# Kernel tuning notes

Measured on AMD Instinct MI355X. Metric: run time of the kernel, lower is better.

The kernel has to match this reference:

```python
import jax, jax.numpy as jnp
import numpy as np

M, C, K, D = 2048, 16, 8, 256  # queries, classes, clusters/class, feature_dim
H1, H2 = D, D // 2             # MLP hidden sizes


def setup_inputs() -> dict:
    key = jax.random.key(0)
    ks = jax.random.split(key, 8)
    s1 = 1.0 / np.sqrt(2 * D)
    s2 = 1.0 / np.sqrt(H1)
    s3 = 1.0 / np.sqrt(H2)
    return {
        "query_features": jax.random.normal(ks[0], (M, D), jnp.float32),
        "prototypes": jax.random.normal(ks[1], (C, K, D), jnp.float32),
        "W1": jax.random.normal(ks[2], (2 * D, H1), jnp.float32) * s1,
        "b1": jnp.zeros((H1,), jnp.float32),
        "W2": jax.random.normal(ks[3], (H1, H2), jnp.float32) * s2,
        "b2": jnp.zeros((H2,), jnp.float32),
        "W3": jax.random.normal(ks[4], (H2, 1), jnp.float32) * s3,
        "b3": jnp.zeros((1,), jnp.float32),
    }


def reference(query_features, prototypes, W1, b1, W2, b2, W3, b3):
    # Attention MLP on concat([query, prototype]) for every (query, class, cluster)
    # pair. Split W1 into the query half and prototype half so we never
    # materialize the [M,C,K,2D] concat; broadcast-add instead.
    d = query_features.shape[-1]
    Wq, Wp = W1[:d], W1[d:]
    qh = query_features @ Wq                      # [M, H1]
    ph = jnp.einsum('ckd,dh->ckh', prototypes, Wp)  # [C, K, H1]
    h = jax.nn.relu(qh[:, None, None, :] + ph[None] + b1)   # [M, C, K, H1]
    h = jax.nn.relu(h @ W2 + b2)                              # [M, C, K, H2]
    scores = (h @ W3)[..., 0] + b3[0]                         # [M, C, K]
    attn = jax.nn.softmax(scores, axis=-1)                    # softmax over clusters
    weighted = jnp.einsum('mck,ckd->mcd', attn, prototypes)   # [M, C, D]
    diff = query_features[:, None, :] - weighted              # [M, C, D]
    distances = jnp.sqrt(jnp.sum(diff * diff, axis=-1))       # [M, C]
    return -distances
```

## Files before the change

kernel.cpp:

```cpp
#include <hip/hip_runtime.h>
#include <hip/hip_fp16.h>
#include <cstdint>

typedef __attribute__((ext_vector_type(8))) _Float16 f16x8;
typedef __attribute__((ext_vector_type(4))) float f32x4;
typedef __attribute__((ext_vector_type(16))) float f32x16;

__device__ __forceinline__ f16x8 cvt8(float4 x, float4 y) {
    f16x8 r;
    r[0] = (_Float16)x.x; r[1] = (_Float16)x.y; r[2] = (_Float16)x.z; r[3] = (_Float16)x.w;
    r[4] = (_Float16)y.x; r[5] = (_Float16)y.y; r[6] = (_Float16)y.z; r[7] = (_Float16)y.w;
    return r;
}

__device__ __forceinline__ f16x8 relu8(f16x8 v) {
    f16x8 z = {};
    return __builtin_elementwise_max(v, z);
}

__global__ __launch_bounds__(256)
void xpose(const float* __restrict__ query,
           const float* __restrict__ prot,
           const float* __restrict__ W1,
           const float* __restrict__ W2,
           const float* __restrict__ b2,
           _Float16* __restrict__ w1t,
           f16x8* __restrict__ w2p,
           float* __restrict__ Gm,
           float* __restrict__ q2) {
    int b = blockIdx.x, t = threadIdx.x;
    if (b < 32) {
        __shared__ _Float16 lt[64][73];
        int bi = b >> 2, bj = b & 3;
        int r0 = bi * 64, c0 = bj * 64;
        #pragma unroll
        for (int it = 0; it < 4; ++it) {
            int row = it * 16 + (t >> 4);
            int c4 = (t & 15) * 4;
            float4 v = *(const float4*)(W1 + (r0 + row) * 256 + c0 + c4);
            lt[row][c4]     = (_Float16)v.x;
            lt[row][c4 + 1] = (_Float16)v.y;
            lt[row][c4 + 2] = (_Float16)v.z;
            lt[row][c4 + 3] = (_Float16)v.w;
        }
        __syncthreads();
        int c = t >> 2, kq = t & 3;
        unsigned short o[16];
        #pragma unroll
        for (int i = 0; i < 16; ++i) {
            union { _Float16 f; unsigned short s; } u;
            u.f = lt[kq * 16 + i][c];
            o[i] = u.s;
        }
        _Float16* dst = w1t + (r0 >= 256 ? 65536 : 0) + (c0 + c) * 256 + (r0 & 255) + kq * 16;
        *(uint4*)dst       = *(uint4*)&o[0];
        *(uint4*)(dst + 8) = *(uint4*)&o[8];
    } else if (b < 49) {
        int chunk = (b - 32) * 256 + t;
        int ks = chunk >> 8, h = (chunk >> 7) & 1, c = chunk & 127;
        f16x8 o = {};
        if (ks < 16) {
            #pragma unroll
            for (int j = 0; j < 8; ++j)
                o[j] = (_Float16)W2[(ks * 16 + h * 8 + j) * 128 + c];
        } else if (h == 0) {
            o[0] = (_Float16)b2[c];
        }
        w2p[chunk] = o;
    } else if (b < 81) {
        int pid = (b - 49) * 32 + (t >> 3), l8 = t & 7;
        int c = pid >> 6, k = (pid >> 3) & 7, kp = pid & 7;
        const float4* pa = (const float4*)(prot + (c * 8 + k) * 256 + l8 * 32);
        const float4* pb = (const float4*)(prot + (c * 8 + kp) * 256 + l8 * 32);
        float s = 0.f;
        #pragma unroll
        for (int i = 0; i < 8; ++i) {
            float4 x = pa[i], y = pb[i];
            s += x.x * y.x + x.y * y.y + x.z * y.z + x.w * y.w;
        }
        s += __shfl_xor(s, 1); s += __shfl_xor(s, 2); s += __shfl_xor(s, 4);
        if (l8 == 0) Gm[pid] = s;
    } else {
        int m = (b - 81) * 32 + (t >> 3), l8 = t & 7;
        const float4* qp = (const float4*)(query + m * 256 + l8 * 32);
        float s = 0.f;
        #pragma unroll
        for (int i = 0; i < 8; ++i) {
            float4 x = qp[i];
            s += x.x * x.x + x.y * x.y + x.z * x.z + x.w * x.w;
        }
        s += __shfl_xor(s, 1); s += __shfl_xor(s, 2); s += __shfl_xor(s, 4);
        if (l8 == 0) q2[m] = s;
    }
}

__global__ __launch_bounds__(256, 2)
void prepg(const float* __restrict__ query,
           const float* __restrict__ prot,
           const _Float16* __restrict__ w1t,
           const float* __restrict__ b1,
           _Float16* __restrict__ qh16,
           float* __restrict__ sqp,
           _Float16* __restrict__ phpk) {
    int b = blockIdx.x, t = threadIdx.x;
    int w = t >> 6, l = t & 63, l15 = l & 15, l4 = l >> 4;
    int mode, row0, col0;
    if (b < 128)      { mode = 0; row0 = (b >> 2) * 64;         col0 = (b & 3) * 64; }
    else if (b < 192) { mode = 1; row0 = ((b - 128) >> 1) * 64; col0 = ((b - 128) & 1) * 64; }
    else              { mode = 2; row0 = ((b - 192) >> 2) * 64; col0 = ((b - 192) & 3) * 64; }
    const float* Asrc = (mode == 2) ? prot : query;
    const _Float16* Bsrc = (mode == 2) ? (w1t + 65536) : w1t;

    f32x4 acc[4];
    #pragma unroll
    for (int nt = 0; nt < 4; ++nt) acc[nt] = (f32x4){0.f, 0.f, 0.f, 0.f};

    for (int ks = 0; ks < 8; ++ks) {
        int row = row0 + w * 16 + l15;
        const float* ap = Asrc + row * 256 + ks * 32 + l4 * 8;
        f16x8 af = cvt8(*(const float4*)ap, *(const float4*)(ap + 4));
        f16x8 bf[4];
        #pragma unroll
        for (int nt = 0; nt < 4; ++nt) {
            int col = col0 + nt * 16 + l15;
            if (mode == 1) {
                const float* bp = prot + col * 256 + ks * 32 + l4 * 8;
                bf[nt] = cvt8(*(const float4*)bp, *(const float4*)(bp + 4));
            } else {
                bf[nt] = *(const f16x8*)(Bsrc + col * 256 + ks * 32 + l4 * 8);
            }
        }
        #pragma unroll
        for (int nt = 0; nt < 4; ++nt)
            acc[nt] = __builtin_amdgcn_mfma_f32_16x16x32_f16(af, bf[nt], acc[nt], 0, 0, 0);
    }
    #pragma unroll
    for (int nt = 0; nt < 4; ++nt)
        #pragma unroll
        for (int j = 0; j < 4; ++j) {
            int row = row0 + w * 16 + l4 * 4 + j;
            int col = col0 + nt * 16 + l15;
            float v = acc[nt][j];
            if (mode == 0)      qh16[row * 256 + col] = (_Float16)v;
            else if (mode == 1) sqp[row * 128 + col] = v;
            else                phpk[(((col >> 4) * 2 + ((col >> 3) & 1)) * 128 + row) * 8
                                     + (col & 7)] = (_Float16)(v + b1[col]);
        }
}

__global__ __launch_bounds__(512, 1)
void fused2(const _Float16* __restrict__ qh16,
            const _Float16* __restrict__ phpk,
            const uint4* __restrict__ w2p,
            const float* __restrict__ sqp,
            const float* __restrict__ q2,
            const float* __restrict__ Gm,
            const float* __restrict__ W3,
            float* __restrict__ out) {
    __shared__ uint4 w2l[4352];
    __shared__ float w3l[128];
    __shared__ float spart[2][2][2][128];

    int t = threadIdx.x;
    int wid = t >> 6, l = t & 63;
    int rg = wid & 3, cs = wid >> 2;
    int lk = l & 31, h = l >> 5;
    int ck = rg * 32 + lk;

    for (int i = t; i < 4352; i += 512) w2l[i] = w2p[i];
    if (t < 128) w3l[t] = W3[t];

    f16x8 ph[16];
    #pragma unroll
    for (int ks = 0; ks < 16; ++ks)
        ph[ks] = *(const f16x8*)(phpk + ((ks * 2 + h) * 128 + ck) * 8);

    __syncthreads();

    const _Float16* w2lh = (const _Float16*)w2l;
    int m0 = blockIdx.x * 8;

    for (int mi = 0; mi < 4; ++mi) {
        int mA = m0 + mi * 2;
        const _Float16* qra = qh16 + mA * 256 + h * 8;
        const _Float16* qrb = qra + 256;

        f32x16 acc[2][2];
        #pragma unroll
        for (int mm = 0; mm < 2; ++mm)
            #pragma unroll
            for (int ct = 0; ct < 2; ++ct) acc[mm][ct] = (f32x16){};

        f16x8 qa[4], qb[4];
        #pragma unroll
        for (int p = 0; p < 4; ++p) {
            qa[p] = *(const f16x8*)(qra + p * 16);
            qb[p] = *(const f16x8*)(qrb + p * 16);
        }

        #pragma unroll
        for (int ks = 0; ks < 16; ++ks) {
            f16x8 aA = relu8(qa[ks & 3] + ph[ks]);
            f16x8 aB = relu8(qb[ks & 3] + ph[ks]);
            if (ks < 12) {
                qa[ks & 3] = *(const f16x8*)(qra + (ks + 4) * 16);
                qb[ks & 3] = *(const f16x8*)(qrb + (ks + 4) * 16);
            }
            #pragma unroll
            for (int ct = 0; ct < 2; ++ct) {
                f16x8 bfr = *(const f16x8*)(w2lh + ((ks * 2 + h) * 128 + cs * 64 + ct * 32 + lk) * 8);
                acc[0][ct] = __builtin_amdgcn_mfma_f32_32x32x16_f16(bfr, aA, acc[0][ct], 0, 0, 0);
                acc[1][ct] = __builtin_amdgcn_mfma_f32_32x32x16_f16(bfr, aB, acc[1][ct], 0, 0, 0);
            }
        }
        {
            f16x8 e = {};
            if (h == 0) e[0] = (_Float16)1.0f;
            #pragma unroll
            for (int ct = 0; ct < 2; ++ct) {
                f16x8 bfr = *(const f16x8*)(w2lh + ((32 + h) * 128 + cs * 64 + ct * 32 + lk) * 8);
                acc[0][ct] = __builtin_amdgcn_mfma_f32_32x32x16_f16(bfr, e, acc[0][ct], 0, 0, 0);
                acc[1][ct] = __builtin_amdgcn_mfma_f32_32x32x16_f16(bfr, e, acc[1][ct], 0, 0, 0);
            }
        }

        int buf = mi & 1;
        #pragma unroll
        for (int mm = 0; mm < 2; ++mm) {
            float s = 0.f;
            #pragma unroll
            for (int ct = 0; ct < 2; ++ct)
                #pragma unroll
                for (int r = 0; r < 16; ++r)
                    s = fmaf(fmaxf(acc[mm][ct][r], 0.f),
                             w3l[cs * 64 + ct * 32 + (r & 3) + 8 * (r >> 2) + 4 * h], s);
            s += __shfl_xor(s, 32);
            if (l < 32) spart[buf][mm][cs][ck] = s;
        }
        __syncthreads();

        if (t < 256) {
            int msel = t >> 7, ckk = t & 127, kk = t & 7;
            int m = mA + msel;
            int c = ckk >> 3;
            float s = spart[buf][msel][0][ckk] + spart[buf][msel][1][ckk];
            float mx = s;
            mx = fmaxf(mx, __shfl_xor(mx, 1));
            mx = fmaxf(mx, __shfl_xor(mx, 2));
            mx = fmaxf(mx, __shfl_xor(mx, 4));
            float e = __expf(s - mx);
            float den = e;
            den += __shfl_xor(den, 1); den += __shfl_xor(den, 2); den += __shfl_xor(den, 4);
            float a = e / den;
            float p2 = a * sqp[m * 128 + ckk];
            float p3 = 0.f;
            #pragma unroll
            for (int kq = 0; kq < 8; ++kq) {
                float ak = __shfl(a, (l & 56) | kq);
                p3 = fmaf(ak, Gm[c * 64 + kq * 8 + kk], p3);
            }
            p3 *= a;
            float pr = p3 - 2.f * p2;
            pr += __shfl_xor(pr, 1); pr += __shfl_xor(pr, 2); pr += __shfl_xor(pr, 4);
            if (kk == 0)
                out[m * 16 + c] = -sqrtf(fmaxf(q2[m] + pr, 0.f));
        }
    }
}

extern "C" void kernel_launch(void* const* d_in, const int* in_sizes, int n_in,
                              void* d_out, int out_size, void* d_ws, size_t ws_size,
                              hipStream_t stream) {
    const float* query = (const float*)d_in[0];
    const float* prot  = (const float*)d_in[1];
    const float* W1    = (const float*)d_in[2];
    const float* b1    = (const float*)d_in[3];
    const float* W2    = (const float*)d_in[4];
    const float* b2    = (const float*)d_in[5];
    const float* W3    = (const float*)d_in[6];

    char* ws = (char*)d_ws;
    _Float16* qh16 = (_Float16*)(ws);
    _Float16* w1t  = (_Float16*)(ws + 1048576);
    f16x8*    w2p  = (f16x8*)(ws + 1310720);
    _Float16* phpk = (_Float16*)(ws + 1380352);
    float*    sqp  = (float*)(ws + 1445888);
    float*    q2   = (float*)(ws + 2494464);
    float*    Gm   = (float*)(ws + 2502656);
    float* out = (float*)d_out;

    xpose<<<145, 256, 0, stream>>>(query, prot, W1, W2, b2, w1t, w2p, Gm, q2);
    prepg<<<200, 256, 0, stream>>>(query, prot, w1t, b1, qh16, sqp, phpk);
    fused2<<<256, 512, 0, stream>>>(qh16, phpk, (const uint4*)w2p,
                                    sqp, q2, Gm, W3, out);
}
```

Measured before the change: 47.18 us.

## Merge three kernels into one cooperative kernel with grid-wide syncs

Combines the preprocessing, projection GEMM and fused MLP/softmax/distance kernels into a single cooperative kernel launched with 256 blocks of 512 threads. Each block runs two former 256-thread work units side by side in the first two phases, and grid.sync() separates the phases. Shared memory is reused across phases through a union. The goal is to remove the launch and drain gaps between kernels. The cost is two grid-wide barriers, and the early phases now run under the register budget of the 512-thread MLP phase.

Result: slower. 114.9 us (+143.6%).

```diff
diff --git a/kernel.cpp b/kernel.cpp
--- a/kernel.cpp
+++ b/kernel.cpp
@@ -1,6 +1,9 @@
 #include <hip/hip_runtime.h>
 #include <hip/hip_fp16.h>
+#include <hip/hip_cooperative_groups.h>
 #include <cstdint>
+
+namespace cg = cooperative_groups;
 
 typedef __attribute__((ext_vector_type(8))) _Float16 f16x8;
 typedef __attribute__((ext_vector_type(4))) float f32x4;
@@ -18,252 +21,253 @@
     return __builtin_elementwise_max(v, z);
 }
 
-__global__ __launch_bounds__(256)
-void xpose(const float* __restrict__ query,
-           const float* __restrict__ prot,
-           const float* __restrict__ W1,
-           const float* __restrict__ W2,
-           const float* __restrict__ b2,
-           _Float16* __restrict__ w1t,
-           f16x8* __restrict__ w2p,
-           float* __restrict__ Gm,
-           float* __restrict__ q2) {
-    int b = blockIdx.x, t = threadIdx.x;
-    if (b < 32) {
-        __shared__ _Float16 lt[64][73];
-        int bi = b >> 2, bj = b & 3;
-        int r0 = bi * 64, c0 = bj * 64;
+__global__ __launch_bounds__(512, 1)
+void mega(const float* __restrict__ query, const float* __restrict__ prot,
+          const float* __restrict__ W1, const float* __restrict__ b1,
+          const float* __restrict__ W2, const float* __restrict__ b2,
+          const float* __restrict__ W3,
+          _Float16* __restrict__ qh16, _Float16* __restrict__ w1t,
+          uint4* __restrict__ w2p, _Float16* __restrict__ phpk,
+          float* __restrict__ sqp, float* __restrict__ q2,
+          float* __restrict__ Gm, float* __restrict__ out)
+{
+    __shared__ union SMem {
+        struct { _Float16 lt[2][64][73]; } a;
+        struct { uint4 w2l[4352]; float w3l[128]; float spart[2][2][2][128]; } c;
+    } sm;
+
+    cg::grid_group grid = cg::this_grid();
+    const int t = threadIdx.x;
+
+    {
+        int u = (int)blockIdx.x * 2 + (t >> 8);
+        int tt = t & 255;
+        if (u < 32) {
+            _Float16 (*lt)[73] = sm.a.lt[t >> 8];
+            int bi = u >> 2, bj = u & 3;
+            int r0 = bi * 64, c0 = bj * 64;
+            #pragma unroll
+            for (int it = 0; it < 4; ++it) {
+                int row = it * 16 + (tt >> 4);
+                int c4 = (tt & 15) * 4;
+                float4 v = *(const float4*)(W1 + (r0 + row) * 256 + c0 + c4);
+                lt[row][c4]     = (_Float16)v.x;
+                lt[row][c4 + 1] = (_Float16)v.y;
+                lt[row][c4 + 2] = (_Float16)v.z;
+                lt[row][c4 + 3] = (_Float16)v.w;
+            }
+            __syncthreads();
+            int c = tt >> 2, kq = tt & 3;
+            unsigned short o[16];
+            #pragma unroll
+            for (int i = 0; i < 16; ++i) {
+                union { _Float16 f; unsigned short s; } uu;
+                uu.f = lt[kq * 16 + i][c];
+                o[i] = uu.s;
+            }
+            _Float16* dst = w1t + (r0 >= 256 ? 65536 : 0) + (c0 + c) * 256 + (r0 & 255) + kq * 16;
+            *(uint4*)dst       = *(uint4*)&o[0];
+            *(uint4*)(dst + 8) = *(uint4*)&o[8];
+        } else if (u < 49) {
+            int chunk = (u - 32) * 256 + tt;
+            int ks = chunk >> 8, h = (chunk >> 7) & 1, c = chunk & 127;
+            f16x8 o = {};
+            if (ks < 16) {
+                #pragma unroll
+                for (int j = 0; j < 8; ++j)
+                    o[j] = (_Float16)W2[(ks * 16 + h * 8 + j) * 128 + c];
+            } else if (h == 0) {
+                o[0] = (_Float16)b2[c];
+            }
+            ((f16x8*)w2p)[chunk] = o;
+        } else if (u < 81) {
+            int pid = (u - 49) * 32 + (tt >> 3), l8 = tt & 7;
+            int c = pid >> 6, k = (pid >> 3) & 7, kp = pid & 7;
+            const float4* pa = (const float4*)(prot + (c * 8 + k) * 256 + l8 * 32);
+            const float4* pb = (const float4*)(prot + (c * 8 + kp) * 256 + l8 * 32);
+            float s = 0.f;
+            #pragma unroll
+            for (int i = 0; i < 8; ++i) {
+                float4 x = pa[i], y = pb[i];
+                s += x.x * y.x + x.y * y.y + x.z * y.z + x.w * y.w;
+            }
+            s += __shfl_xor(s, 1); s += __shfl_xor(s, 2); s += __shfl_xor(s, 4);
+            if (l8 == 0) Gm[pid] = s;
+        } else if (u < 145) {
+            int m = (u - 81) * 32 + (tt >> 3), l8 = tt & 7;
+            const float4* qp = (const float4*)(query + m * 256 + l8 * 32);
+            float s = 0.f;
+            #pragma unroll
+            for (int i = 0; i < 8; ++i) {
+                float4 x = qp[i];
+                s += x.x * x.x + x.y * x.y + x.z * x.z + x.w * x.w;
+            }
+            s += __shfl_xor(s, 1); s += __shfl_xor(s, 2); s += __shfl_xor(s, 4);
+            if (l8 == 0) q2[m] = s;
+        }
+    }
+
+    grid.sync();
+
+    {
+        int hu = (int)blockIdx.x * 2 + (t >> 8);
+        if (hu < 200) {
+            int tt = t & 255;
+            int w = tt >> 6, l = tt & 63, l15 = l & 15, l4 = l >> 4;
+            int mode, row0, col0;
+            if (hu < 128)      { mode = 0; row0 = (hu >> 2) * 64;         col0 = (hu & 3) * 64; }
+            else if (hu < 192) { mode = 1; row0 = ((hu - 128) >> 1) * 64; col0 = ((hu - 128) & 1) * 64; }
+            else               { mode = 2; row0 = ((hu - 192) >> 2) * 64; col0 = ((hu - 192) & 3) * 64; }
+            const float* Asrc = (mode == 2) ? prot : query;
+            const _Float16* Bsrc = (mode == 2) ? (w1t + 65536) : w1t;
+
+            f32x4 acc[4];
+            #pragma unroll
+            for (int nt = 0; nt < 4; ++nt) acc[nt] = (f32x4){0.f, 0.f, 0.f, 0.f};
+
+            for (int ks = 0; ks < 8; ++ks) {
+                int row = row0 + w * 16 + l15;
+                const float* ap = Asrc + row * 256 + ks * 32 + l4 * 8;
+                f16x8 af = cvt8(*(const float4*)ap, *(const float4*)(ap + 4));
+                f16x8 bf[4];
+                #pragma unroll
+                for (int nt = 0; nt < 4; ++nt) {
+                    int col = col0 + nt * 16 + l15;
+                    if (mode == 1) {
+                        const float* bp = prot + col * 256 + ks * 32 + l4 * 8;
+                        bf[nt] = cvt8(*(const float4*)bp, *(const float4*)(bp + 4));
+                    } else {
+                        bf[nt] = *(const f16x8*)(Bsrc + col * 256 + ks * 32 + l4 * 8);
+                    }
+                }
+                #pragma unroll
+                for (int nt = 0; nt < 4; ++nt)
+                    acc[nt] = __builtin_amdgcn_mfma_f32_16x16x32_f16(af, bf[nt], acc[nt], 0, 0, 0);
+            }
+            #pragma unroll
+            for (int nt = 0; nt < 4; ++nt)
+                #pragma unroll
+                for (int j = 0; j < 4; ++j) {
+                    int row = row0 + w * 16 + l4 * 4 + j;
+                    int col = col0 + nt * 16 + l15;
+                    float v = acc[nt][j];
+                    if (mode == 0)      qh16[row * 256 + col] = (_Float16)v;
+                    else if (mode == 1) sqp[row * 128 + col] = v;
+                    else                phpk[(((col >> 4) * 2 + ((col >> 3) & 1)) * 128 + row) * 8
+                                             + (col & 7)] = (_Float16)(v + b1[col]);
+                }
+        }
+    }
+
+    grid.sync();
+
+    {
+        uint4* w2l = sm.c.w2l;
+        float* w3l = sm.c.w3l;
+
+        int wid = t >> 6, l = t & 63;
+        int rg = wid & 3, cs = wid >> 2;
+        int lk = l & 31, h = l >> 5;
+        int ck = rg * 32 + lk;
+
+        for (int i = t; i < 4352; i += 512) w2l[i] = w2p[i];
+        if (t < 128) w3l[t] = W3[t];
+
+        f16x8 ph[16];
         #pragma unroll
-        for (int it = 0; it < 4; ++it) {
-            int row = it * 16 + (t >> 4);
-            int c4 = (t & 15) * 4;
-            float4 v = *(const float4*)(W1 + (r0 + row) * 256 + c0 + c4);
-            lt[row][c4]     = (_Float16)v.x;
-            lt[row][c4 + 1] = (_Float16)v.y;
-            lt[row][c4 + 2] = (_Float16)v.z;
-            lt[row][c4 + 3] = (_Float16)v.w;
-        }
+        for (int ks = 0; ks < 16; ++ks)
+            ph[ks] = *(const f16x8*)(phpk + ((ks * 2 + h) * 128 + ck) * 8);
+
         __syncthreads();
-        int c = t >> 2, kq = t & 3;
-        unsigned short o[16];
-        #pragma unroll
-        for (int i = 0; i < 16; ++i) {
-            union { _Float16 f; unsigned short s; } u;
-            u.f = lt[kq * 16 + i][c];
-            o[i] = u.s;
-        }
-        _Float16* dst = w1t + (r0 >= 256 ? 65536 : 0) + (c0 + c) * 256 + (r0 & 255) + kq * 16;
-        *(uint4*)dst       = *(uint4*)&o[0];
-        *(uint4*)(dst + 8) = *(uint4*)&o[8];
-    } else if (b < 49) {
-        int chunk = (b - 32) * 256 + t;
-        int ks = chunk >> 8, h = (chunk >> 7) & 1, c = chunk & 127;
-        f16x8 o = {};
-        if (ks < 16) {
-            #pragma unroll
-            for (int j = 0; j < 8; ++j)
-                o[j] = (_Float16)W2[(ks * 16 + h * 8 + j) * 128 + c];
-        } else if (h == 0) {
-            o[0] = (_Float16)b2[c];
-        }
-        w2p[chunk] = o;
-    } else if (b < 81) {
-        int pid = (b - 49) * 32 + (t >> 3), l8 = t & 7;
-        int c = pid >> 6, k = (pid >> 3) & 7, kp = pid & 7;
-        const float4* pa = (const float4*)(prot + (c * 8 + k) * 256 + l8 * 32);
-        const float4* pb = (const float4*)(prot + (c * 8 + kp) * 256 + l8 * 32);
-        float s = 0.f;
-        #pragma unroll
-        for (int i = 0; i < 8; ++i) {
-            float4 x = pa[i], y = pb[i];
-            s += x.x * y.x + x.y * y.y + x.z * y.z + x.w * y.w;
-        }
-        s += __shfl_xor(s, 1); s += __shfl_xor(s, 2); s += __shfl_xor(s, 4);
-        if (l8 == 0) Gm[pid] = s;
-    } else {
-        int m = (b - 81) * 32 + (t >> 3), l8 = t & 7;
-        const float4* qp = (const float4*)(query + m * 256 + l8 * 32);
-        float s = 0.f;
-        #pragma unroll
-        for (int i = 0; i < 8; ++i) {
-            float4 x = qp[i];
-            s += x.x * x.x + x.y * x.y + x.z * x.z + x.w * x.w;
-        }
-        s += __shfl_xor(s, 1); s += __shfl_xor(s, 2); s += __shfl_xor(s, 4);
-        if (l8 == 0) q2[m] = s;
-    }
-}
-
-__global__ __launch_bounds__(256, 2)
-void prepg(const float* __restrict__ query,
-           const float* __restrict__ prot,
-           const _Float16* __restrict__ w1t,
-           const float* __restrict__ b1,
-           _Float16* __restrict__ qh16,
-           float* __restrict__ sqp,
-           _Float16* __restrict__ phpk) {
-    int b = blockIdx.x, t = threadIdx.x;
-    int w = t >> 6, l = t & 63, l15 = l & 15, l4 = l >> 4;
-    int mode, row0, col0;
-    if (b < 128)      { mode = 0; row0 = (b >> 2) * 64;         col0 = (b & 3) * 64; }
-    else if (b < 192) { mode = 1; row0 = ((b - 128) >> 1) * 64; col0 = ((b - 128) & 1) * 64; }
-    else              { mode = 2; row0 = ((b - 192) >> 2) * 64; col0 = ((b - 192) & 3) * 64; }
-    const float* Asrc = (mode == 2) ? prot : query;
-    const _Float16* Bsrc = (mode == 2) ? (w1t + 65536) : w1t;
-
-    f32x4 acc[4];
-    #pragma unroll
-    for (int nt = 0; nt < 4; ++nt) acc[nt] = (f32x4){0.f, 0.f, 0.f, 0.f};
-
-    for (int ks = 0; ks < 8; ++ks) {
-        int row = row0 + w * 16 + l15;
-        const float* ap = Asrc + row * 256 + ks * 32 + l4 * 8;
-        f16x8 af = cvt8(*(const float4*)ap, *(const float4*)(ap + 4));
-        f16x8 bf[4];
-        #pragma unroll
-        for (int nt = 0; nt < 4; ++nt) {
-            int col = col0 + nt * 16 + l15;
-            if (mode == 1) {
-                const float* bp = prot + col * 256 + ks * 32 + l4 * 8;
-                bf[nt] = cvt8(*(const float4*)bp, *(const float4*)(bp + 4));
-            } else {
-                bf[nt] = *(const f16x8*)(Bsrc + col * 256 + ks * 32 + l4 * 8);
-            }
-        }
-        #pragma unroll
-        for (int nt = 0; nt < 4; ++nt)
-            acc[nt] = __builtin_amdgcn_mfma_f32_16x16x32_f16(af, bf[nt], acc[nt], 0, 0, 0);
-    }
-    #pragma unroll
-    for (int nt = 0; nt < 4; ++nt)
-        #pragma unroll
-        for (int j = 0; j < 4; ++j) {
-            int row = row0 + w * 16 + l4 * 4 + j;
-            int col = col0 + nt * 16 + l15;
-            float v = acc[nt][j];
-            if (mode == 0)      qh16[row * 256 + col] = (_Float16)v;
-            else if (mode == 1) sqp[row * 128 + col] = v;
-            else                phpk[(((col >> 4) * 2 + ((col >> 3) & 1)) * 128 + row) * 8
-                                     + (col & 7)] = (_Float16)(v + b1[col]);
-        }
-}
-
-__global__ __launch_bounds__(512, 1)
-void fused2(const _Float16* __restrict__ qh16,
-            const _Float16* __restrict__ phpk,
-            const uint4* __restrict__ w2p,
-            const float* __restrict__ sqp,
-            const float* __restrict__ q2,
-            const float* __restrict__ Gm,
-            const float* __restrict__ W3,
-            float* __restrict__ out) {
-    __shared__ uint4 w2l[4352];
-    __shared__ float w3l[128];
-    __shared__ float spart[2][2][2][128];
-
-    int t = threadIdx.x;
-    int wid = t >> 6, l = t & 63;
-    int rg = wid & 3, cs = wid >> 2;
-    int lk = l & 31, h = l >> 5;
-    int ck = rg * 32 + lk;
-
-    for (int i = t; i < 4352; i += 512) w2l[i] = w2p[i];
-    if (t < 128) w3l[t] = W3[t];
-
-    f16x8 ph[16];
-    #pragma unroll
-    for (int ks = 0; ks < 16; ++ks)
-        ph[ks] = *(const f16x8*)(phpk + ((ks * 2 + h) * 128 + ck) * 8);
-
-    __syncthreads();
-
-    const _Float16* w2lh = (const _Float16*)w2l;
-    int m0 = blockIdx.x * 8;
-
-    for (int mi = 0; mi < 4; ++mi) {
-        int mA = m0 + mi * 2;
-        const _Float16* qra = qh16 + mA * 256 + h * 8;
-        const _Float16* qrb = qra + 256;
-
-        f32x16 acc[2][2];
-        #pragma unroll
-        for (int mm = 0; mm < 2; ++mm)
-            #pragma unroll
-            for (int ct = 0; ct < 2; ++ct) acc[mm][ct] = (f32x16){};
-
-        f16x8 qa[4], qb[4];
-        #pragma unroll
-        for (int p = 0; p < 4; ++p) {
-            qa[p] = *(const f16x8*)(qra + p * 16);
-            qb[p] = *(const f16x8*)(qrb + p * 16);
-        }
-
-        #pragma unroll
-        for (int ks = 0; ks < 16; ++ks) {
-            f16x8 aA = relu8(qa[ks & 3] + ph[ks]);
-            f16x8 aB = relu8(qb[ks & 3] + ph[ks]);
-            if (ks < 12) {
-                qa[ks & 3] = *(const f16x8*)(qra + (ks + 4) * 16);
-                qb[ks & 3] = *(const f16x8*)(qrb + (ks + 4) * 16);
-            }
-            #pragma unroll
-            for (int ct = 0; ct < 2; ++ct) {
-                f16x8 bfr = *(const f16x8*)(w2lh + ((ks * 2 + h) * 128 + cs * 64 + ct * 32 + lk) * 8);
-                acc[0][ct] = __builtin_amdgcn_mfma_f32_32x32x16_f16(bfr, aA, acc[0][ct], 0, 0, 0);
-                acc[1][ct] = __builtin_amdgcn_mfma_f32_32x32x16_f16(bfr, aB, acc[1][ct], 0, 0, 0);
-            }
-        }
-        {
-            f16x8 e = {};
-            if (h == 0) e[0] = (_Float16)1.0f;
-            #pragma unroll
-            for (int ct = 0; ct < 2; ++ct) {
-                f16x8 bfr = *(const f16x8*)(w2lh + ((32 + h) * 128 + cs * 64 + ct * 32 + lk) * 8);
-                acc[0][ct] = __builtin_amdgcn_mfma_f32_32x32x16_f16(bfr, e, acc[0][ct], 0, 0, 0);
-                acc[1][ct] = __builtin_amdgcn_mfma_f32_32x32x16_f16(bfr, e, acc[1][ct], 0, 0, 0);
-            }
-        }
-
-        int buf = mi & 1;
-        #pragma unroll
-        for (int mm = 0; mm < 2; ++mm) {
-            float s = 0.f;
-            #pragma unroll
-            for (int ct = 0; ct < 2; ++ct)
-                #pragma unroll
-                for (int r = 0; r < 16; ++r)
-                    s = fmaf(fmaxf(acc[mm][ct][r], 0.f),
-                             w3l[cs * 64 + ct * 32 + (r & 3) + 8 * (r >> 2) + 4 * h], s);
-            s += __shfl_xor(s, 32);
-            if (l < 32) spart[buf][mm][cs][ck] = s;
-        }
-        __syncthreads();
-
-        if (t < 256) {
-            int msel = t >> 7, ckk = t & 127, kk = t & 7;
-            int m = mA + msel;
-            int c = ckk >> 3;
-            float s = spart[buf][msel][0][ckk] + spart[buf][msel][1][ckk];
-            float mx = s;
-            mx = fmaxf(mx, __shfl_xor(mx, 1));
-            mx = fmaxf(mx, __shfl_xor(mx, 2));
-            mx = fmaxf(mx, __shfl_xor(mx, 4));
-            float e = __expf(s - mx);
-            float den = e;
-            den += __shfl_xor(den, 1); den += __shfl_xor(den, 2); den += __shfl_xor(den, 4);
-            float a = e / den;
-            float p2 = a * sqp[m * 128 + ckk];
-            float p3 = 0.f;
-            #pragma unroll
-            for (int kq = 0; kq < 8; ++kq) {
-                float ak = __shfl(a, (l & 56) | kq);
-                p3 = fmaf(ak, Gm[c * 64 + kq * 8 + kk], p3);
-            }
-            p3 *= a;
-            float pr = p3 - 2.f * p2;
-            pr += __shfl_xor(pr, 1); pr += __shfl_xor(pr, 2); pr += __shfl_xor(pr, 4);
-            if (kk == 0)
-                out[m * 16 + c] = -sqrtf(fmaxf(q2[m] + pr, 0.f));
+
+        const _Float16* w2lh = (const _Float16*)w2l;
+        int m0 = blockIdx.x * 8;
+
+        for (int mi = 0; mi < 4; ++mi) {
+            int mA = m0 + mi * 2;
+            const _Float16* qra = qh16 + mA * 256 + h * 8;
+            const _Float16* qrb = qra + 256;
+
+            f32x16 acc[2][2];
+            #pragma unroll
+            for (int mm = 0; mm < 2; ++mm)
+                #pragma unroll
+                for (int ct = 0; ct < 2; ++ct) acc[mm][ct] = (f32x16){};
+
+            f16x8 qa[4], qb[4];
+            #pragma unroll
+            for (int p = 0; p < 4; ++p) {
+                qa[p] = *(const f16x8*)(qra + p * 16);
+                qb[p] = *(const f16x8*)(qrb + p * 16);
+            }
+
+            #pragma unroll
+            for (int ks = 0; ks < 16; ++ks) {
+                f16x8 aA = relu8(qa[ks & 3] + ph[ks]);
+                f16x8 aB = relu8(qb[ks & 3] + ph[ks]);
+                if (ks < 12) {
+                    qa[ks & 3] = *(const f16x8*)(qra + (ks + 4) * 16);
+                    qb[ks & 3] = *(const f16x8*)(qrb + (ks + 4) * 16);
+                }
+                #pragma unroll
+                for (int ct = 0; ct < 2; ++ct) {
+                    f16x8 bfr = *(const f16x8*)(w2lh + ((ks * 2 + h) * 128 + cs * 64 + ct * 32 + lk) * 8);
+                    acc[0][ct] = __builtin_amdgcn_mfma_f32_32x32x16_f16(bfr, aA, acc[0][ct], 0, 0, 0);
+                    acc[1][ct] = __builtin_amdgcn_mfma_f32_32x32x16_f16(bfr, aB, acc[1][ct], 0, 0, 0);
+                }
+            }
+            {
+                f16x8 e = {};
+                if (h == 0) e[0] = (_Float16)1.0f;
+                #pragma unroll
+                for (int ct = 0; ct < 2; ++ct) {
+                    f16x8 bfr = *(const f16x8*)(w2lh + ((32 + h) * 128 + cs * 64 + ct * 32 + lk) * 8);
+                    acc[0][ct] = __builtin_amdgcn_mfma_f32_32x32x16_f16(bfr, e, acc[0][ct], 0, 0, 0);
+                    acc[1][ct] = __builtin_amdgcn_mfma_f32_32x32x16_f16(bfr, e, acc[1][ct], 0, 0, 0);
+                }
+            }
+
+            int buf = mi & 1;
+            #pragma unroll
+            for (int mm = 0; mm < 2; ++mm) {
+                float s = 0.f;
+                #pragma unroll
+                for (int ct = 0; ct < 2; ++ct)
+                    #pragma unroll
+                    for (int r = 0; r < 16; ++r)
+                        s = fmaf(fmaxf(acc[mm][ct][r], 0.f),
+                                 w3l[cs * 64 + ct * 32 + (r & 3) + 8 * (r >> 2) + 4 * h], s);
+                s += __shfl_xor(s, 32);
+                if (l < 32) sm.c.spart[buf][mm][cs][ck] = s;
+            }
+            __syncthreads();
+
+            if (t < 256) {
+                int msel = t >> 7, ckk = t & 127, kk = t & 7;
+                int m = mA + msel;
+                int c = ckk >> 3;
+                float s = sm.c.spart[buf][msel][0][ckk] + sm.c.spart[buf][msel][1][ckk];
+                float mx = s;
+                mx = fmaxf(mx, __shfl_xor(mx, 1));
+                mx = fmaxf(mx, __shfl_xor(mx, 2));
+                mx = fmaxf(mx, __shfl_xor(mx, 4));
+                float e = __expf(s - mx);
+                float den = e;
+                den += __shfl_xor(den, 1); den += __shfl_xor(den, 2); den += __shfl_xor(den, 4);
+                float a = e / den;
+                float p2 = a * sqp[m * 128 + ckk];
+                float p3 = 0.f;
+                #pragma unroll
+                for (int kq = 0; kq < 8; ++kq) {
+                    float ak = __shfl(a, (l & 56) | kq);
+                    p3 = fmaf(ak, Gm[c * 64 + kq * 8 + kk], p3);
+                }
+                p3 *= a;
+                float pr = p3 - 2.f * p2;
+                pr += __shfl_xor(pr, 1); pr += __shfl_xor(pr, 2); pr += __shfl_xor(pr, 4);
+                if (kk == 0)
+                    out[m * 16 + c] = -sqrtf(fmaxf(q2[m] + pr, 0.f));
+            }
         }
     }
 }
@@ -282,15 +286,16 @@
     char* ws = (char*)d_ws;
     _Float16* qh16 = (_Float16*)(ws);
     _Float16* w1t  = (_Float16*)(ws + 1048576);
-    f16x8*    w2p  = (f16x8*)(ws + 1310720);
+    uint4*    w2p  = (uint4*)(ws + 1310720);
     _Float16* phpk = (_Float16*)(ws + 1380352);
     float*    sqp  = (float*)(ws + 1445888);
     float*    q2   = (float*)(ws + 2494464);
     float*    Gm   = (float*)(ws + 2502656);
-    float* out = (float*)d_out;
-
-    xpose<<<145, 256, 0, stream>>>(query, prot, W1, W2, b2, w1t, w2p, Gm, q2);
-    prepg<<<200, 256, 0, stream>>>(query, prot, w1t, b1, qh16, sqp, phpk);
-    fused2<<<256, 512, 0, stream>>>(qh16, phpk, (const uint4*)w2p,
-                                    sqp, q2, Gm, W3, out);
+    float*    out  = (float*)d_out;
+
+    void* args[] = { (void*)&query, (void*)&prot, (void*)&W1, (void*)&b1,
+                     (void*)&W2, (void*)&b2, (void*)&W3,
+                     (void*)&qh16, (void*)&w1t, (void*)&w2p, (void*)&phpk,
+                     (void*)&sqp, (void*)&q2, (void*)&Gm, (void*)&out };
+    (void)hipLaunchCooperativeKernel((const void*)mega, dim3(256), dim3(512), args, 0, stream);
 }
```

## Double fused kernel block to 1024 threads and stage prototype hidden in LDS

Applied to the files above, without the earlier changes.

The fused MLP kernel now runs 16 waves per block instead of 8. Each wave computes a 32-column slice of the second layer rather than 64, which halves the accumulator registers per wave. The prototype hidden activations move from 16 per-thread registers into shared memory (64 KB more LDS) and are read per k-step. This trades register pressure for more waves to hide latency, at the cost of extra LDS reads, a larger shared-memory footprint, and a four-way partial-score reduction.

Measured after the change: 47.71 us. About the same (+1.1%).

```diff
diff --git a/kernel.cpp b/kernel.cpp
--- a/kernel.cpp
+++ b/kernel.cpp
@@ -148,9 +148,9 @@
         }
 }
 
-__global__ __launch_bounds__(512, 1)
-void fused2(const _Float16* __restrict__ qh16,
-            const _Float16* __restrict__ phpk,
+__global__ __launch_bounds__(1024, 1)
+void fused3(const _Float16* __restrict__ qh16,
+            const uint4* __restrict__ phpk,
             const uint4* __restrict__ w2p,
             const float* __restrict__ sqp,
             const float* __restrict__ q2,
@@ -158,8 +158,9 @@
             const float* __restrict__ W3,
             float* __restrict__ out) {
     __shared__ uint4 w2l[4352];
+    __shared__ uint4 phl[4096];
     __shared__ float w3l[128];
-    __shared__ float spart[2][2][2][128];
+    __shared__ float spart[2][2][4][128];
 
     int t = threadIdx.x;
     int wid = t >> 6, l = t & 63;
@@ -167,17 +168,13 @@
     int lk = l & 31, h = l >> 5;
     int ck = rg * 32 + lk;
 
-    for (int i = t; i < 4352; i += 512) w2l[i] = w2p[i];
+    for (int i = t; i < 4352; i += 1024) w2l[i] = w2p[i];
+    for (int i = t; i < 4096; i += 1024) phl[i] = phpk[i];
     if (t < 128) w3l[t] = W3[t];
-
-    f16x8 ph[16];
-    #pragma unroll
-    for (int ks = 0; ks < 16; ++ks)
-        ph[ks] = *(const f16x8*)(phpk + ((ks * 2 + h) * 128 + ck) * 8);
-
     __syncthreads();
 
     const _Float16* w2lh = (const _Float16*)w2l;
+    const _Float16* phlh = (const _Float16*)phl;
     int m0 = blockIdx.x * 8;
 
     for (int mi = 0; mi < 4; ++mi) {
@@ -185,65 +182,70 @@
         const _Float16* qra = qh16 + mA * 256 + h * 8;
         const _Float16* qrb = qra + 256;
 
-        f32x16 acc[2][2];
-        #pragma unroll
-        for (int mm = 0; mm < 2; ++mm)
-            #pragma unroll
-            for (int ct = 0; ct < 2; ++ct) acc[mm][ct] = (f32x16){};
-
-        f16x8 qa[4], qb[4];
-        #pragma unroll
-        for (int p = 0; p < 4; ++p) {
-            qa[p] = *(const f16x8*)(qra + p * 16);
-            qb[p] = *(const f16x8*)(qrb + p * 16);
-        }
+        f32x16 accA = {}, accB = {};
+
+        f16x8 qa[2], qb[2];
+        qa[0] = *(const f16x8*)(qra);
+        qb[0] = *(const f16x8*)(qrb);
+        qa[1] = *(const f16x8*)(qra + 16);
+        qb[1] = *(const f16x8*)(qrb + 16);
 
         #pragma unroll
         for (int ks = 0; ks < 16; ++ks) {
-            f16x8 aA = relu8(qa[ks & 3] + ph[ks]);
-            f16x8 aB = relu8(qb[ks & 3] + ph[ks]);
-            if (ks < 12) {
-                qa[ks & 3] = *(const f16x8*)(qra + (ks + 4) * 16);
-                qb[ks & 3] = *(const f16x8*)(qrb + (ks + 4) * 16);
-            }
-            #pragma unroll
-            for (int ct = 0; ct < 2; ++ct) {
-                f16x8 bfr = *(const f16x8*)(w2lh + ((ks * 2 + h) * 128 + cs * 64 + ct * 32 + lk) * 8);
-                acc[0][ct] = __builtin_amdgcn_mfma_f32_32x32x16_f16(bfr, aA, acc[0][ct], 0, 0, 0);
-                acc[1][ct] = __builtin_amdgcn_mfma_f32_32x32x16_f16(bfr, aB, acc[1][ct], 0, 0, 0);
-            }
+            f16x8 ph = *(const f16x8*)(phlh + ((ks * 2 + h) * 128 + ck) * 8);
+            f16x8 aA = relu8(qa[ks & 1] + ph);
+            f16x8 aB = relu8(qb[ks & 1] + ph);
+            if (ks < 14) {
+                qa[ks & 1] = *(const f16x8*)(qra + (ks + 2) * 16);
+                qb[ks & 1] = *(const f16x8*)(qrb + (ks + 2) * 16);
+            }
+            f16x8 bfr = *(const f16x8*)(w2lh + ((ks * 2 + h) * 128 + cs * 32 + lk) * 8);
+            accA = __builtin_amdgcn_mfma_f32_32x32x16_f16(bfr, aA, accA, 0, 0, 0);
+            accB = __builtin_amdgcn_mfma_f32_32x32x16_f16(bfr, aB, accB, 0, 0, 0);
         }
         {
             f16x8 e = {};
             if (h == 0) e[0] = (_Float16)1.0f;
-            #pragma unroll
-            for (int ct = 0; ct < 2; ++ct) {
-                f16x8 bfr = *(const f16x8*)(w2lh + ((32 + h) * 128 + cs * 64 + ct * 32 + lk) * 8);
-                acc[0][ct] = __builtin_amdgcn_mfma_f32_32x32x16_f16(bfr, e, acc[0][ct], 0, 0, 0);
-                acc[1][ct] = __builtin_amdgcn_mfma_f32_32x32x16_f16(bfr, e, acc[1][ct], 0, 0, 0);
-            }
+            f16x8 bfr = *(const f16x8*)(w2lh + ((32 + h) * 128 + cs * 32 + lk) * 8);
+            accA = __builtin_amdgcn_mfma_f32_32x32x16_f16(bfr, e, accA, 0, 0, 0);
+            accB = __builtin_amdgcn_mfma_f32_32x32x16_f16(bfr, e, accB, 0, 0, 0);
         }
 
         int buf = mi & 1;
-        #pragma unroll
-        for (int mm = 0; mm < 2; ++mm) {
-            float s = 0.f;
-            #pragma unroll
-            for (int ct = 0; ct < 2; ++ct)
-                #pragma unroll
-                for (int r = 0; r < 16; ++r)
-                    s = fmaf(fmaxf(acc[mm][ct][r], 0.f),
-                             w3l[cs * 64 + ct * 32 + (r & 3) + 8 * (r >> 2) + 4 * h], s);
+        {
+            float s0 = 0.f, s1 = 0.f, s2 = 0.f, s3 = 0.f;
+            #pragma unroll
+            for (int r = 0; r < 16; r += 4) {
+                s0 = fmaf(fmaxf(accA[r + 0], 0.f), w3l[cs * 32 + ((r + 0) & 3) + 8 * ((r + 0) >> 2) + 4 * h], s0);
+                s1 = fmaf(fmaxf(accA[r + 1], 0.f), w3l[cs * 32 + ((r + 1) & 3) + 8 * ((r + 1) >> 2) + 4 * h], s1);
+                s2 = fmaf(fmaxf(accA[r + 2], 0.f), w3l[cs * 32 + ((r + 2) & 3) + 8 * ((r + 2) >> 2) + 4 * h], s2);
+                s3 = fmaf(fmaxf(accA[r + 3], 0.f), w3l[cs * 32 + ((r + 3) & 3) + 8 * ((r + 3) >> 2) + 4 * h], s3);
+            }
+            float s = (s0 + s1) + (s2 + s3);
             s += __shfl_xor(s, 32);
-            if (l < 32) spart[buf][mm][cs][ck] = s;
+            if (l < 32) spart[buf][0][cs][ck] = s;
+        }
+        {
+            float s0 = 0.f, s1 = 0.f, s2 = 0.f, s3 = 0.f;
+            #pragma unroll
+            for (int r = 0; r < 16; r += 4) {
+                s0 = fmaf(fmaxf(accB[r + 0], 0.f), w3l[cs * 32 + ((r + 0) & 3) + 8 * ((r + 0) >> 2) + 4 * h], s0);
+                s1 = fmaf(fmaxf(accB[r + 1], 0.f), w3l[cs * 32 + ((r + 1) & 3) + 8 * ((r + 1) >> 2) + 4 * h], s1);
+                s2 = fmaf(fmaxf(accB[r + 2], 0.f), w3l[cs * 32 + ((r + 2) & 3) + 8 * ((r + 2) >> 2) + 4 * h], s2);
+                s3 = fmaf(fmaxf(accB[r + 3], 0.f), w3l[cs * 32 + ((r + 3) & 3) + 8 * ((r + 3) >> 2) + 4 * h], s3);
+            }
+            float s = (s0 + s1) + (s2 + s3);
+            s += __shfl_xor(s, 32);
+            if (l < 32) spart[buf][1][cs][ck] = s;
         }
         __syncthreads();
 
         if (t < 256) {
             int msel = t >> 7, ckk = t & 127, kk = t & 7;
             int m = mA + msel;
-            int c = ckk >> 3;
-            float s = spart[buf][msel][0][ckk] + spart[buf][msel][1][ckk];
+            int cg = ckk >> 3;
+            float s = spart[buf][msel][0][ckk] + spart[buf][msel][1][ckk]
+                    + spart[buf][msel][2][ckk] + spart[buf][msel][3][ckk];
             float mx = s;
             mx = fmaxf(mx, __shfl_xor(mx, 1));
             mx = fmaxf(mx, __shfl_xor(mx, 2));
@@ -257,13 +259,13 @@
             #pragma unroll
             for (int kq = 0; kq < 8; ++kq) {
                 float ak = __shfl(a, (l & 56) | kq);
-                p3 = fmaf(ak, Gm[c * 64 + kq * 8 + kk], p3);
+                p3 = fmaf(ak, Gm[cg * 64 + kq * 8 + kk], p3);
             }
             p3 *= a;
             float pr = p3 - 2.f * p2;
             pr += __shfl_xor(pr, 1); pr += __shfl_xor(pr, 2); pr += __shfl_xor(pr, 4);
             if (kk == 0)
-                out[m * 16 + c] = -sqrtf(fmaxf(q2[m] + pr, 0.f));
+                out[m * 16 + cg] = -sqrtf(fmaxf(q2[m] + pr, 0.f));
         }
     }
 }
@@ -291,6 +293,6 @@
 
     xpose<<<145, 256, 0, stream>>>(query, prot, W1, W2, b2, w1t, w2p, Gm, q2);
     prepg<<<200, 256, 0, stream>>>(query, prot, w1t, b1, qh16, sqp, phpk);
-    fused2<<<256, 512, 0, stream>>>(qh16, phpk, (const uint4*)w2p,
-                                    sqp, q2, Gm, W3, out);
-}
+    fused3<<<256, 1024, 0, stream>>>(qh16, (const uint4*)phpk, (const uint4*)w2p,
+                                     sqp, q2, Gm, W3, out);
+}
```
